# Performance work log

Measured on AMD Instinct MI355X. Metric: run time of the kernel, lower is better.

The kernel has to match this reference:

```python
import jax, jax.numpy as jnp
import numpy as np
from jax import lax

DIM, GC1, GC2, GC3 = 128, 32, 64, 32
B, H, W = 4, 128, 128
EPS = 1e-5


def conv2d(x, w, b, pad, dilation=1, groups=1):
    y = lax.conv_general_dilated(x, w, (1, 1), [(pad, pad), (pad, pad)],
                                 rhs_dilation=(dilation, dilation),
                                 feature_group_count=groups,
                                 dimension_numbers=('NCHW', 'OIHW', 'NCHW'))
    return y + b[None, :, None, None]


def bilinear_gather(img, ys, xs):
    # img [B,C,H,W]; ys,xs [B,K,H,W] float sample coords. Zero padding outside.
    b, c, h, w = img.shape
    k = ys.shape[1]
    flat = img.reshape(b, c, h * w)
    y0 = jnp.floor(ys)
    x0 = jnp.floor(xs)
    acc = jnp.zeros((b, c, k, h, w), img.dtype)
    for dy in (0, 1):
        for dx in (0, 1):
            yc = y0 + dy
            xc = x0 + dx
            wgt = (1.0 - jnp.abs(ys - yc)) * (1.0 - jnp.abs(xs - xc))
            valid = (yc >= 0) & (yc <= h - 1) & (xc >= 0) & (xc <= w - 1)
            yi = jnp.clip(yc, 0, h - 1).astype(jnp.int32)
            xi = jnp.clip(xc, 0, w - 1).astype(jnp.int32)
            idx = (yi * w + xi).reshape(b, 1, k * h * w)
            g = jnp.take_along_axis(flat, jnp.broadcast_to(idx, (b, c, k * h * w)), axis=2)
            g = g.reshape(b, c, k, h, w)
            acc = acc + g * (wgt * valid.astype(img.dtype))[:, None]
    return acc


def deform_depthwise(x, off, w):
    # x [B,C,H,W], off [B,2*9,H,W] (dy,dx interleaved per kernel tap), w [C,9]
    b, c, h, ww = x.shape
    off = off.reshape(b, 9, 2, h, ww)
    dy, dx = off[:, :, 0], off[:, :, 1]  # [B,9,H,W]
    ks = jnp.arange(3, dtype=x.dtype)
    kyy = jnp.repeat(ks, 3)  # [9]
    kxx = jnp.tile(ks, 3)
    iy = jnp.arange(h, dtype=x.dtype)
    jx = jnp.arange(ww, dtype=x.dtype)
    ys = iy[None, None, :, None] - 1.0 + kyy[None, :, None, None] + dy
    xs = jx[None, None, None, :] - 1.0 + kxx[None, :, None, None] + dx
    sampled = bilinear_gather(x, ys, xs)  # [B,C,9,H,W]
    return jnp.einsum('bckhw,ck->bchw', sampled, w)


def batchnorm(x, g, b):
    mu = jnp.mean(x, axis=(0, 2, 3), keepdims=True)
    var = jnp.var(x, axis=(0, 2, 3), keepdims=True)
    return (x - mu) * lax.rsqrt(var + EPS) * g[None, :, None, None] + b[None, :, None, None]


def setup_inputs() -> dict:
    key = jax.random.key(0)
    ks = jax.random.split(key, 16)
    s = 0.05
    return {
        'x': jax.random.normal(ks[0], (B, DIM, H, W), jnp.float32),
        'offset_w': jax.random.normal(ks[1], (18, GC1, 3, 3), jnp.float32) * s,
        'offset_b': jax.random.normal(ks[2], (18,), jnp.float32) * s,
        'deform_w': jax.random.normal(ks[3], (GC1, 9), jnp.float32) * s,
        'dw_w': jax.random.normal(ks[4], (GC2, 1, 7, 7), jnp.float32) * s,
        'dw_b': jax.random.normal(ks[5], (GC2,), jnp.float32) * s,
        'dw2_w': jax.random.normal(ks[6], (GC3, GC3, 3, 3), jnp.float32) * s,
        'dw2_b': jax.random.normal(ks[7], (GC3,), jnp.float32) * s,
        'bn1_g': jnp.ones((DIM,), jnp.float32),
        'bn1_b': jnp.zeros((DIM,), jnp.float32),
        'w1': jax.random.normal(ks[8], (DIM, 4 * DIM), jnp.float32) * s,
        'b1': jax.random.normal(ks[9], (4 * DIM,), jnp.float32) * s,
        'w2': jax.random.normal(ks[10], (4 * DIM, DIM), jnp.float32) * s,
        'b2': jax.random.normal(ks[11], (DIM,), jnp.float32) * s,
        'bn2_g': jnp.ones((DIM,), jnp.float32),
        'bn2_b': jnp.zeros((DIM,), jnp.float32),
    }


def reference(x, offset_w, offset_b, deform_w, dw_w, dw_b, dw2_w, dw2_b,
              bn1_g, bn1_b, w1, b1, w2, b2, bn2_g, bn2_b):
    x_hw, x_w, x_h = jnp.split(x, [GC1, GC1 + GC2], axis=1)
    off = conv2d(x_hw, offset_w, offset_b, pad=1)
    d0 = deform_depthwise(x_hw, off, deform_w)
    d1 = conv2d(x_w, dw_w, dw_b, pad=3, groups=GC2)          # 7x7 depthwise
    d2 = conv2d(x_h, dw2_w, dw2_b, pad=2, dilation=2)        # 3x3 dense, dilation 2
    y = jnp.concatenate([d0, d1, d2], axis=1)
    # channel shuffle, groups=2
    b, c, h, w = y.shape
    y = y.reshape(b, 2, c // 2, h, w).transpose(0, 2, 1, 3, 4).reshape(b, c, h, w)
    y = batchnorm(y, bn1_g, bn1_b)
    t = y.transpose(0, 2, 3, 1)                               # [B,H,W,C]
    t = jax.nn.gelu(t @ w1 + b1, approximate=False)
    t = t @ w2 + b2
    y = t.transpose(0, 3, 1, 2)
    y = batchnorm(y, bn2_g, bn2_b)
    return jax.nn.gelu(x + y, approximate=False)
```

## Files before the change

kernel.cpp:

```cpp
#include <hip/hip_runtime.h>
#include <hip/hip_bf16.h>
#include <math.h>

#define BB 4
#define CC 128
#define HH 128
#define WWD 128
#define HWW 16384
#define PREC 17424

typedef __attribute__((ext_vector_type(8))) short bf16x8;
typedef __attribute__((ext_vector_type(4))) float floatx4;
typedef __attribute__((ext_vector_type(4))) unsigned short us4;
typedef __attribute__((ext_vector_type(8))) unsigned short us8;

__device__ __forceinline__ float gelu_fast(float v) {
  float u = v * v;
  float z = v * fmaf(0.0713548163f, u, 1.5957691216f);
  float e = __builtin_amdgcn_exp2f(-1.4426950409f * z);
  return v * __builtin_amdgcn_rcpf(1.0f + e);
}
__device__ __forceinline__ unsigned short f2us(float f) {
  union { float f; unsigned int u; } c; c.f = f;
  unsigned int u = c.u;
  return (unsigned short)((u + 0x7FFFu + ((u >> 16) & 1u)) >> 16);
}

__global__ __launch_bounds__(256) void k_zero(
    unsigned short* __restrict__ xp, float* __restrict__ part2) {
  if (blockIdx.x == 33) { part2[threadIdx.x] = 0.f; return; }
  int g = blockIdx.x * 256 + threadIdx.x;
  if (g >= 8320) return;
  int pl = g / 1040;
  int r = g - pl * 1040;
  int yy, xx;
  if (r < 528) {
    int q = r / 132;
    yy = q < 2 ? q : 126 + q;
    xx = r - q * 132;
  } else {
    int r2 = r - 528;
    yy = 2 + (r2 >> 2);
    int side = r2 & 3;
    xx = side < 2 ? side : 128 + side;
  }
  long rec = (long)pl * PREC + yy * 132 + xx;
  unsigned short* d = &xp[rec * 32];
  us8 z = (us8)0;
  *(us8*)&d[0] = z; *(us8*)&d[8] = z; *(us8*)&d[16] = z; *(us8*)&d[24] = z;
}

__global__ __launch_bounds__(256) void k_pack(
    const float* __restrict__ x, unsigned short* __restrict__ xp,
    float* __restrict__ xt) {
  __shared__ float t[64 * 33];
  int bid = blockIdx.x;
  int tid = threadIdx.x;
  int which = bid >> 10, b = (bid >> 8) & 3, pg = bid & 255;
  int cbase = which ? 96 : 0;
  int c = tid >> 3, g8 = tid & 7;
  const float* xpr = x + ((long)b * CC + cbase + c) * HWW + pg * 64 + g8 * 8;
  float4 v0 = *(const float4*)xpr;
  float4 v1 = *(const float4*)(xpr + 4);
  t[(g8 * 8 + 0) * 33 + c] = v0.x; t[(g8 * 8 + 1) * 33 + c] = v0.y;
  t[(g8 * 8 + 2) * 33 + c] = v0.z; t[(g8 * 8 + 3) * 33 + c] = v0.w;
  t[(g8 * 8 + 4) * 33 + c] = v1.x; t[(g8 * 8 + 5) * 33 + c] = v1.y;
  t[(g8 * 8 + 6) * 33 + c] = v1.z; t[(g8 * 8 + 7) * 33 + c] = v1.w;
  __syncthreads();
  int u = tid >> 2, q = tid & 3;
  int p = pg * 64 + u;
  int yy = p >> 7, xx = p & 127;
  long rec = (long)(which * 4 + b) * PREC + (yy + 2) * 132 + xx + 2;
  us8 o;
  float vv[8];
#pragma unroll
  for (int k = 0; k < 8; k++) {
    vv[k] = t[u * 33 + q * 8 + k];
    o[k] = f2us(vv[k]);
  }
  *(us8*)&xp[rec * 32 + q * 8] = o;
  if (which == 0) {
    float* d = xt + ((long)b * HWW + p) * 32 + q * 8;
    float4 o0, o1;
    o0.x = vv[0]; o0.y = vv[1]; o0.z = vv[2]; o0.w = vv[3];
    o1.x = vv[4]; o1.y = vv[5]; o1.z = vv[6]; o1.w = vv[7];
    *(float4*)d = o0;
    *(float4*)(d + 4) = o1;
  }
}

__global__ __launch_bounds__(256) void k_wprep2(
    const float* __restrict__ offw, const float* __restrict__ dilw,
    unsigned short* __restrict__ wob, unsigned short* __restrict__ w3b) {
  int t = blockIdx.x * 256 + threadIdx.x;
  if (t >= 2304) return;
  int which = t >= 1152;
  int u = t - which * 1152;
  int lane = u & 63, tn = u >> 6;
  int col = lane & 15, quad = lane >> 4;
  int tap = tn >> 1, nt = tn & 1;
  int n = nt * 16 + col;
  const float* W = which ? dilw : offw;
  int noc = which ? 32 : 18;
  unsigned short* d = (which ? w3b : wob) + (long)(tn * 64 + lane) * 8;
#pragma unroll
  for (int j = 0; j < 8; j++)
    d[j] = (n < noc) ? f2us(W[(long)n * 288 + (quad * 8 + j) * 9 + tap]) : (unsigned short)0;
}

__global__ __launch_bounds__(256) void k_offc_mm(
    const unsigned short* __restrict__ xp0, const unsigned short* __restrict__ wob,
    const float* __restrict__ bias, float* __restrict__ off) {
  int bid = blockIdx.x;
  int b = bid >> 7, yy = bid & 127;
  int tid = threadIdx.x;
  int lane = tid & 63, wv = tid >> 6;
  int row = lane & 15, quad = lane >> 4;
  const unsigned short* plane = xp0 + (long)b * PREC * 32;
  int xb = wv * 32;
  floatx4 Oa[2][2];
#pragma unroll
  for (int mt = 0; mt < 2; mt++)
#pragma unroll
    for (int nt = 0; nt < 2; nt++) Oa[mt][nt] = (floatx4)0.f;
#pragma unroll
  for (int t = 0; t < 9; t++) {
    int dy = t / 3 - 1, dx = t % 3 - 1;
    const unsigned short* rp = plane + ((long)(yy + 2 + dy) * 132 + 2 + dx + xb) * 32;
    bf16x8 A0 = *(const bf16x8*)&rp[row * 32 + quad * 8];
    bf16x8 A1 = *(const bf16x8*)&rp[(16 + row) * 32 + quad * 8];
#pragma unroll
    for (int nt = 0; nt < 2; nt++) {
      bf16x8 Bf = *(const bf16x8*)&wob[(long)((t * 2 + nt) * 64 + lane) * 8];
      Oa[0][nt] = __builtin_amdgcn_mfma_f32_16x16x32_bf16(A0, Bf, Oa[0][nt], 0, 0, 0);
      Oa[1][nt] = __builtin_amdgcn_mfma_f32_16x16x32_bf16(A1, Bf, Oa[1][nt], 0, 0, 0);
    }
  }
#pragma unroll
  for (int nt = 0; nt < 2; nt++) {
    int oc = nt * 16 + (lane & 15);
    if (oc < 18) {
      float bb = bias[oc];
#pragma unroll
      for (int mt = 0; mt < 2; mt++) {
        floatx4 v = Oa[mt][nt];
        v[0] += bb; v[1] += bb; v[2] += bb; v[3] += bb;
        long p = (long)(b * 18 + oc) * HWW + yy * 128 + xb + mt * 16 + quad * 4;
        *(floatx4*)&off[p] = v;
      }
    }
  }
}

__global__ __launch_bounds__(256) void k_dil3_mm(
    const unsigned short* __restrict__ xp1, const unsigned short* __restrict__ w3b,
    const float* __restrict__ bias, float* __restrict__ y) {
  int bid = blockIdx.x;
  int b = bid >> 7, yy = bid & 127;
  int tid = threadIdx.x;
  int lane = tid & 63, wv = tid >> 6;
  int row = lane & 15, quad = lane >> 4;
  const unsigned short* plane = xp1 + (long)b * PREC * 32;
  int xb = wv * 32;
  floatx4 Oa[2][2];
#pragma unroll
  for (int mt = 0; mt < 2; mt++)
#pragma unroll
    for (int nt = 0; nt < 2; nt++) Oa[mt][nt] = (floatx4)0.f;
#pragma unroll
  for (int t = 0; t < 9; t++) {
    int dy = (t / 3 - 1) * 2, dx = (t % 3 - 1) * 2;
    const unsigned short* rp = plane + ((long)(yy + 2 + dy) * 132 + 2 + dx + xb) * 32;
    bf16x8 A0 = *(const bf16x8*)&rp[row * 32 + quad * 8];
    bf16x8 A1 = *(const bf16x8*)&rp[(16 + row) * 32 + quad * 8];
#pragma unroll
    for (int nt = 0; nt < 2; nt++) {
      bf16x8 Bf = *(const bf16x8*)&w3b[(long)((t * 2 + nt) * 64 + lane) * 8];
      Oa[0][nt] = __builtin_amdgcn_mfma_f32_16x16x32_bf16(A0, Bf, Oa[0][nt], 0, 0, 0);
      Oa[1][nt] = __builtin_amdgcn_mfma_f32_16x16x32_bf16(A1, Bf, Oa[1][nt], 0, 0, 0);
    }
  }
#pragma unroll
  for (int nt = 0; nt < 2; nt++) {
    int oc = nt * 16 + (lane & 15);
    int cp = 65 + 2 * oc;
    float bb = bias[oc];
#pragma unroll
    for (int mt = 0; mt < 2; mt++) {
      floatx4 v = Oa[mt][nt];
      v[0] += bb; v[1] += bb; v[2] += bb; v[3] += bb;
      long p = ((long)b * CC + cp) * HWW + yy * 128 + xb + mt * 16 + quad * 4;
      *(floatx4*)&y[p] = v;
    }
  }
}

__global__ __launch_bounds__(256) void k_deform(
    const float* __restrict__ xt, const float* __restrict__ off,
    const float* __restrict__ dw, float* __restrict__ y) {
  __shared__ float wl[144];
  int tid = threadIdx.x;
  int g = blockIdx.x * 256 + tid;
  int hf = g >> 16;
  int pix = g & 65535;
  if (tid < 144) {
    int k = tid >> 4, q = tid & 15;
    wl[k * 16 + q] = dw[(hf * 16 + q) * 9 + k];
  }
  __syncthreads();
  int b = pix >> 14, p = pix & 16383;
  int i = p >> 7, j = p & 127;
  float acc[16];
#pragma unroll
  for (int q = 0; q < 16; q++) acc[q] = 0.f;
  const float* offb = off + (long)b * 18 * HWW + p;
  const float* xb = xt + (long)b * HWW * 32 + hf * 16;
  for (int k = 0; k < 9; k++) {
    float dy = offb[(long)(2 * k) * HWW];
    float dx = offb[(long)(2 * k + 1) * HWW];
    float ys = (float)i - 1.f + (float)(k / 3) + dy;
    float xs = (float)j - 1.f + (float)(k % 3) + dx;
    float y0 = floorf(ys), x0 = floorf(xs);
    float fy = ys - y0, fx = xs - x0;
    int iy0 = (int)y0, ix0 = (int)x0;
    int iy1 = iy0 + 1, ix1 = ix0 + 1;
    float wy0 = (1.f - fy) * ((iy0 >= 0 && iy0 <= 127) ? 1.f : 0.f);
    float wy1 = fy * ((iy1 >= 0 && iy1 <= 127) ? 1.f : 0.f);
    float wx0 = (1.f - fx) * ((ix0 >= 0 && ix0 <= 127) ? 1.f : 0.f);
    float wx1 = fx * ((ix1 >= 0 && ix1 <= 127) ? 1.f : 0.f);
    int cy0 = min(max(iy0, 0), 127), cy1 = min(max(iy1, 0), 127);
    int cx0 = min(max(ix0, 0), 127), cx1 = min(max(ix1, 0), 127);
    int ci[4] = {cy0 * 128 + cx0, cy0 * 128 + cx1, cy1 * 128 + cx0, cy1 * 128 + cx1};
    float cw[4] = {wy0 * wx0, wy0 * wx1, wy1 * wx0, wy1 * wx1};
    float v[16];
#pragma unroll
    for (int q = 0; q < 16; q++) v[q] = 0.f;
#pragma unroll
    for (int cn = 0; cn < 4; cn++) {
      const float* cp = xb + (long)ci[cn] * 32;
      float wc = cw[cn];
      float4 p0 = *(const float4*)cp;
      float4 p1 = *(const float4*)(cp + 4);
      float4 p2 = *(const float4*)(cp + 8);
      float4 p3 = *(const float4*)(cp + 12);
      v[0] += wc * p0.x;  v[1] += wc * p0.y;  v[2] += wc * p0.z;  v[3] += wc * p0.w;
      v[4] += wc * p1.x;  v[5] += wc * p1.y;  v[6] += wc * p1.z;  v[7] += wc * p1.w;
      v[8] += wc * p2.x;  v[9] += wc * p2.y;  v[10] += wc * p2.z; v[11] += wc * p2.w;
      v[12] += wc * p3.x; v[13] += wc * p3.y; v[14] += wc * p3.z; v[15] += wc * p3.w;
    }
    const float* wr = &wl[k * 16];
#pragma unroll
    for (int q = 0; q < 16; q++) acc[q] += wr[q] * v[q];
  }
#pragma unroll
  for (int q = 0; q < 16; q++) {
    int cp = 2 * (hf * 16 + q);
    y[((long)b * CC + cp) * HWW + p] = acc[q];
  }
}

__global__ __launch_bounds__(256) void k_dw7(
    const float* __restrict__ x, const float* __restrict__ w,
    const float* __restrict__ bias, float* __restrict__ y) {
  __shared__ float tile[22 * 136];
  __shared__ float wl[49];
  __shared__ float bsh;
  int bid = blockIdx.x;
  int b = bid >> 9, m = (bid >> 3) & 63, strip = bid & 7;
  int r0 = strip * 16;
  int tid = threadIdx.x;
  const float* xp = x + ((long)b * CC + 32 + m) * HWW;
  for (int idx = tid; idx < 2948; idx += 256) {
    int rr = idx / 134;
    int cc = idx - rr * 134 - 3;
    int gy = r0 - 3 + rr;
    float v = 0.f;
    if ((unsigned)gy < 128u && (unsigned)cc < 128u) v = xp[gy * 128 + cc];
    tile[rr * 136 + cc + 3] = v;
  }
  if (tid < 49) wl[tid] = w[m * 49 + tid];
  if (tid == 64) bsh = bias[m];
  __syncthreads();
  int j = tid & 127, s = tid >> 7;
  float acc[8];
#pragma unroll
  for (int o = 0; o < 8; o++) acc[o] = bsh;
#pragma unroll
  for (int kx = 0; kx < 7; kx++) {
#pragma unroll
    for (int rr = 0; rr < 14; rr++) {
      float v = tile[(s * 8 + rr) * 136 + j + kx];
      int olo = rr - 6 > 0 ? rr - 6 : 0;
      int ohi = rr < 7 ? rr : 7;
#pragma unroll
      for (int o = 0; o < 8; o++) {
        if (o >= olo && o <= ohi) acc[o] += v * wl[(rr - o) * 7 + kx];
      }
    }
  }
  int c = 32 + m;
  int cp = (c & 63) * 2 + (c >> 6);
  float* yp = y + ((long)b * CC + cp) * HWW;
#pragma unroll
  for (int o = 0; o < 8; o++) {
    yp[(r0 + s * 8 + o) * 128 + j] = acc[o];
  }
}

__global__ __launch_bounds__(256) void k_stats1(
    const float* __restrict__ buf, float* __restrict__ part) {
  __shared__ float sh[256], sh2[256];
  int c = blockIdx.x >> 2, b = blockIdx.x & 3;
  int tid = threadIdx.x;
  const float* p = buf + ((long)b * CC + c) * HWW;
  float s = 0.f, s2 = 0.f;
  for (int it = 0; it < 16; it++) {
    float4 v = *(const float4*)(p + (it * 256 + tid) * 4);
    s += v.x + v.y + v.z + v.w;
    s2 += v.x * v.x + v.y * v.y + v.z * v.z + v.w * v.w;
  }
  sh[tid] = s; sh2[tid] = s2;
  __syncthreads();
  for (int o = 128; o > 0; o >>= 1) {
    if (tid < o) { sh[tid] += sh[tid + o]; sh2[tid] += sh2[tid + o]; }
    __syncthreads();
  }
  if (tid == 0) {
    part[blockIdx.x * 2] = sh[0];
    part[blockIdx.x * 2 + 1] = sh2[0];
  }
}

__global__ __launch_bounds__(128) void k_stats2(
    const float* __restrict__ part, float* __restrict__ mean, float* __restrict__ istd) {
  int c = threadIdx.x;
  float s = 0.f, s2 = 0.f;
#pragma unroll
  for (int b = 0; b < 4; b++) {
    s += part[(c * 4 + b) * 2];
    s2 += part[(c * 4 + b) * 2 + 1];
  }
  float mu = s * (1.f / 65536.f);
  float var = s2 * (1.f / 65536.f) - mu * mu;
  mean[c] = mu;
  istd[c] = rsqrtf(var + 1e-5f);
}

__global__ __launch_bounds__(128) void k_stats2b(
    const float* __restrict__ part2, float* __restrict__ mean, float* __restrict__ istd) {
  int c = threadIdx.x;
  float mu = part2[c] * (1.f / 65536.f);
  float var = part2[128 + c] * (1.f / 65536.f) - mu * mu;
  mean[c] = mu;
  istd[c] = rsqrtf(var + 1e-5f);
}

__global__ __launch_bounds__(256) void k_wprep(
    const float* __restrict__ w1, const float* __restrict__ w2,
    unsigned short* __restrict__ w1b, unsigned short* __restrict__ w2b) {
  int t = blockIdx.x * 256 + threadIdx.x;
  int which = t >> 13;
  int u = t & 8191;
  int lane = u & 63;
  int ntks = u >> 6;
  int col = lane & 15, quad = lane >> 4;
  if (which == 0) {
    int nt = ntks >> 2, ks = ntks & 3;
    int n = nt * 16 + col;
    int k0 = ks * 32 + quad * 8;
    unsigned short* d = w1b + (long)u * 8;
#pragma unroll
    for (int j = 0; j < 8; j++) d[j] = f2us(w1[(long)(k0 + j) * 512 + n]);
  } else {
    int nt = ntks >> 4, ks = ntks & 15;
    int n = nt * 16 + col;
    int k0 = ks * 32 + quad * 8;
    unsigned short* d = w2b + (long)u * 8;
#pragma unroll
    for (int j = 0; j < 8; j++) d[j] = f2us(w2[(long)(k0 + j) * 128 + n]);
  }
}

__global__ __launch_bounds__(256, 2) void k_mlp_mfma(
    const float* __restrict__ y, const float* __restrict__ mean1,
    const float* __restrict__ istd1, const float* __restrict__ g1,
    const float* __restrict__ b1n, const unsigned short* __restrict__ w1b,
    const float* __restrict__ b1, const unsigned short* __restrict__ w2b,
    const float* __restrict__ b2, float* __restrict__ tmid,
    float* __restrict__ part2) {
  __shared__ unsigned short At[128 * 136];
  __shared__ unsigned short Hs[4 * 32 * 72];
  __shared__ float scs[128], shs[128];
  __shared__ float ps[128], ps2[128];
  int tid = threadIdx.x;
  int lane = tid & 63, wv = tid >> 6;
  int row = lane & 15, quad = lane >> 4;
  int n0 = blockIdx.x * 128;
  int b = n0 >> 14;
  long base = (long)b * CC * HWW + (n0 & 16383);
  if (tid < 128) {
    float sc = istd1[tid] * g1[tid];
    scs[tid] = sc;
    shs[tid] = b1n[tid] - mean1[tid] * sc;
    ps[tid] = 0.f; ps2[tid] = 0.f;
  }
  __syncthreads();
  for (int it = 0; it < 16; it++) {
    int u = it * 256 + tid;
    int tok = u & 127, cg = u >> 7;
    us4 wvv;
#pragma unroll
    for (int r = 0; r < 4; r++) {
      int c = cg * 4 + r;
      float v = y[base + (long)c * HWW + tok];
      wvv[r] = f2us(v * scs[c] + shs[c]);
    }
    *(us4*)&At[tok * 136 + cg * 4] = wvv;
  }
  __syncthreads();
  bf16x8 Af[2][4];
#pragma unroll
  for (int mt = 0; mt < 2; mt++)
#pragma unroll
    for (int ks = 0; ks < 4; ks++)
      Af[mt][ks] = *(const bf16x8*)&At[(wv * 32 + mt * 16 + row) * 136 + ks * 32 + quad * 8];

  floatx4 Oa[2][8];
#pragma unroll
  for (int mt = 0; mt < 2; mt++)
#pragma unroll
    for (int nt = 0; nt < 8; nt++) Oa[mt][nt] = (floatx4)0.f;

  const int wvb = wv * 32 * 72;
  for (int ch = 0; ch < 8; ch++) {
    floatx4 Ha[4][2];
#pragma unroll
    for (int nt = 0; nt < 4; nt++)
#pragma unroll
      for (int mt = 0; mt < 2; mt++) Ha[nt][mt] = (floatx4)0.f;
#pragma unroll
    for (int nt = 0; nt < 4; nt++) {
      int ht = ch * 4 + nt;
#pragma unroll
      for (int ks = 0; ks < 4; ks++) {
        bf16x8 Wf = *(const bf16x8*)&w1b[(long)(((ht * 4 + ks) << 6) + lane) * 8];
        Ha[nt][0] = __builtin_amdgcn_mfma_f32_16x16x32_bf16(Wf, Af[0][ks], Ha[nt][0], 0, 0, 0);
        Ha[nt][1] = __builtin_amdgcn_mfma_f32_16x16x32_bf16(Wf, Af[1][ks], Ha[nt][1], 0, 0, 0);
      }
    }
#pragma unroll
    for (int nt = 0; nt < 4; nt++) {
      float4 bb = *(const float4*)&b1[ch * 64 + nt * 16 + quad * 4];
#pragma unroll
      for (int mt = 0; mt < 2; mt++) {
        us4 hv;
        hv[0] = f2us(gelu_fast(Ha[nt][mt][0] + bb.x));
        hv[1] = f2us(gelu_fast(Ha[nt][mt][1] + bb.y));
        hv[2] = f2us(gelu_fast(Ha[nt][mt][2] + bb.z));
        hv[3] = f2us(gelu_fast(Ha[nt][mt][3] + bb.w));
        *(us4*)&Hs[wvb + (mt * 16 + row) * 72 + nt * 16 + quad * 4] = hv;
      }
    }
    __syncthreads();
    bf16x8 A2[2][2];
#pragma unroll
    for (int mt = 0; mt < 2; mt++)
#pragma unroll
      for (int ks = 0; ks < 2; ks++)
        A2[mt][ks] = *(const bf16x8*)&Hs[wvb + (mt * 16 + row) * 72 + ks * 32 + quad * 8];
#pragma unroll
    for (int nt = 0; nt < 8; nt++) {
#pragma unroll
      for (int ks = 0; ks < 2; ks++) {
        bf16x8 Bf = *(const bf16x8*)&w2b[(long)(((nt * 16 + ch * 2 + ks) << 6) + lane) * 8];
        Oa[0][nt] = __builtin_amdgcn_mfma_f32_16x16x32_bf16(A2[0][ks], Bf, Oa[0][nt], 0, 0, 0);
        Oa[1][nt] = __builtin_amdgcn_mfma_f32_16x16x32_bf16(A2[1][ks], Bf, Oa[1][nt], 0, 0, 0);
      }
    }
    __syncthreads();
  }
#pragma unroll
  for (int nt = 0; nt < 8; nt++) {
    int c = nt * 16 + row;
    float bb = b2[c];
    long op = base + (long)c * HWW + wv * 32 + quad * 4;
    float s = 0.f, s2 = 0.f;
#pragma unroll
    for (int mt = 0; mt < 2; mt++) {
      floatx4 vv = Oa[mt][nt];
      vv[0] += bb; vv[1] += bb; vv[2] += bb; vv[3] += bb;
      *(floatx4*)&tmid[op + mt * 16] = vv;
      s += vv[0] + vv[1] + vv[2] + vv[3];
      s2 += vv[0] * vv[0] + vv[1] * vv[1] + vv[2] * vv[2] + vv[3] * vv[3];
    }
    atomicAdd(&ps[c], s);
    atomicAdd(&ps2[c], s2);
  }
  __syncthreads();
  if (tid < 128) {
    atomicAdd(&part2[tid], ps[tid]);
    atomicAdd(&part2[128 + tid], ps2[tid]);
  }
}

__global__ __launch_bounds__(256) void k_final(
    const float* __restrict__ x, const float* __restrict__ mean2,
    const float* __restrict__ istd2, const float* __restrict__ g2,
    const float* __restrict__ b2n, float* __restrict__ out) {
  long e4 = (long)blockIdx.x * 256 + threadIdx.x;
  int c = (int)((e4 >> 12) & 127);
  float sc = istd2[c] * g2[c];
  float sh = b2n[c] - mean2[c] * sc;
  float4 o = *(float4*)&out[e4 * 4];
  float4 xv = *(const float4*)&x[e4 * 4];
  o.x = gelu_fast(xv.x + o.x * sc + sh);
  o.y = gelu_fast(xv.y + o.y * sc + sh);
  o.z = gelu_fast(xv.z + o.z * sc + sh);
  o.w = gelu_fast(xv.w + o.w * sc + sh);
  *(float4*)&out[e4 * 4] = o;
}

extern "C" void kernel_launch(void* const* d_in, const int* in_sizes, int n_in,
                              void* d_out, int out_size, void* d_ws, size_t ws_size,
                              hipStream_t stream) {
  const float* x        = (const float*)d_in[0];
  const float* offset_w = (const float*)d_in[1];
  const float* offset_b = (const float*)d_in[2];
  const float* deform_w = (const float*)d_in[3];
  const float* dw_w     = (const float*)d_in[4];
  const float* dw_b     = (const float*)d_in[5];
  const float* dw2_w    = (const float*)d_in[6];
  const float* dw2_b    = (const float*)d_in[7];
  const float* bn1_g    = (const float*)d_in[8];
  const float* bn1_b    = (const float*)d_in[9];
  const float* w1       = (const float*)d_in[10];
  const float* b1       = (const float*)d_in[11];
  const float* w2       = (const float*)d_in[12];
  const float* b2       = (const float*)d_in[13];
  const float* bn2_g    = (const float*)d_in[14];
  const float* bn2_b    = (const float*)d_in[15];
  float* out = (float*)d_out;

  float* ws    = (float*)d_ws;
  float* off   = ws;
  float* ybuf  = ws + 1179648;
  float* stats = ws + 9568256;
  float* mean1 = stats, *istd1 = stats + 128;
  float* mean2 = stats + 256, *istd2 = stats + 384;
  unsigned short* w1b = (unsigned short*)(ws + 9568768);
  unsigned short* w2b = (unsigned short*)(ws + 9601536);
  float* part  = ws + 9634304;
  float* xt    = ws + 9635328;
  unsigned short* wob = (unsigned short*)(ws + 11732480);
  unsigned short* w3b = (unsigned short*)(ws + 11737088);
  unsigned short* xp  = (unsigned short*)(ws + 11741696);
  unsigned short* xp0 = xp;
  unsigned short* xp1 = xp + (long)4 * PREC * 32;
  float* part2 = ws + 13971968;
  float* tmid  = out;

  k_zero<<<34, 256, 0, stream>>>(xp, part2);
  k_wprep<<<64, 256, 0, stream>>>(w1, w2, w1b, w2b);
  k_wprep2<<<9, 256, 0, stream>>>(offset_w, dw2_w, wob, w3b);
  k_pack<<<2048, 256, 0, stream>>>(x, xp, xt);
  k_offc_mm<<<512, 256, 0, stream>>>(xp0, wob, offset_b, off);
  k_deform<<<512, 256, 0, stream>>>(xt, off, deform_w, ybuf);
  k_dw7<<<2048, 256, 0, stream>>>(x, dw_w, dw_b, ybuf);
  k_dil3_mm<<<512, 256, 0, stream>>>(xp1, w3b, dw2_b, ybuf);
  k_stats1<<<512, 256, 0, stream>>>(ybuf, part);
  k_stats2<<<1, 128, 0, stream>>>(part, mean1, istd1);
  k_mlp_mfma<<<512, 256, 0, stream>>>(ybuf, mean1, istd1, bn1_g, bn1_b, w1b, b1, w2b, b2, tmid, part2);
  k_stats2b<<<1, 128, 0, stream>>>(part2, mean2, istd2);
  k_final<<<8192, 256, 0, stream>>>(x, mean2, istd2, bn2_g, bn2_b, out);
}
```

Baseline: 278.8 us.

## Split fused MLP kernel into two GEMM kernels with bf16 hidden buffer

Replaces the single fused MLP kernel (both GEMMs with the hidden activation kept in shared memory) with two kernels. The first writes GELU(W1·BN1(y)) to a global bf16 buffer and the second reads it to compute W2 and the BN2 partial stats. This is meant to lower register and LDS pressure per kernel and raise occupancy with smaller 64-token tiles. The cost is an extra 16 MB write and read of the hidden activation, plus a dependency on workspace size, with a fallback to the fused kernel when the workspace is too small.

```diff
diff --git a/kernel.cpp b/kernel.cpp
--- a/kernel.cpp
+++ b/kernel.cpp
@@ -381,6 +381,115 @@
   }
 }
 
+__global__ __launch_bounds__(256) void k_gemm1(
+    const float* __restrict__ y, const float* __restrict__ mean1,
+    const float* __restrict__ istd1, const float* __restrict__ g1,
+    const float* __restrict__ b1n, const unsigned short* __restrict__ w1b,
+    const float* __restrict__ b1, unsigned short* __restrict__ Hbuf) {
+  __shared__ unsigned short At[64 * 136];
+  __shared__ float scs[128], shs[128];
+  int tid = threadIdx.x;
+  int lane = tid & 63, wv = tid >> 6;
+  int row = lane & 15, quad = lane >> 4;
+  int t0 = blockIdx.x * 64;
+  int b = t0 >> 14;
+  long base = (long)b * CC * HWW + (t0 & 16383);
+  if (tid < 128) {
+    float sc = istd1[tid] * g1[tid];
+    scs[tid] = sc;
+    shs[tid] = b1n[tid] - mean1[tid] * sc;
+  }
+  __syncthreads();
+  for (int it = 0; it < 8; it++) {
+    int u = it * 256 + tid;
+    int tok = u & 63, cg = u >> 6;
+    us4 wvv;
+#pragma unroll
+    for (int r = 0; r < 4; r++) {
+      int c = cg * 4 + r;
+      float v = y[base + (long)c * HWW + tok];
+      wvv[r] = f2us(v * scs[c] + shs[c]);
+    }
+    *(us4*)&At[tok * 136 + cg * 4] = wvv;
+  }
+  __syncthreads();
+  bf16x8 Af[4];
+#pragma unroll
+  for (int ks = 0; ks < 4; ks++)
+    Af[ks] = *(const bf16x8*)&At[(wv * 16 + row) * 136 + ks * 32 + quad * 8];
+  long hrow = ((long)(t0 + wv * 16 + row)) * 512;
+  for (int ch = 0; ch < 8; ch++) {
+    floatx4 Ha[4];
+#pragma unroll
+    for (int nt = 0; nt < 4; nt++) Ha[nt] = (floatx4)0.f;
+#pragma unroll
+    for (int nt = 0; nt < 4; nt++) {
+      int ht = ch * 4 + nt;
+#pragma unroll
+      for (int ks = 0; ks < 4; ks++) {
+        bf16x8 Wf = *(const bf16x8*)&w1b[(long)(((ht * 4 + ks) << 6) + lane) * 8];
+        Ha[nt] = __builtin_amdgcn_mfma_f32_16x16x32_bf16(Wf, Af[ks], Ha[nt], 0, 0, 0);
+      }
+    }
+#pragma unroll
+    for (int nt = 0; nt < 4; nt++) {
+      float4 bb = *(const float4*)&b1[ch * 64 + nt * 16 + quad * 4];
+      us4 hv;
+      hv[0] = f2us(gelu_fast(Ha[nt][0] + bb.x));
+      hv[1] = f2us(gelu_fast(Ha[nt][1] + bb.y));
+      hv[2] = f2us(gelu_fast(Ha[nt][2] + bb.z));
+      hv[3] = f2us(gelu_fast(Ha[nt][3] + bb.w));
+      *(us4*)&Hbuf[hrow + ch * 64 + nt * 16 + quad * 4] = hv;
+    }
+  }
+}
+
+__global__ __launch_bounds__(256) void k_gemm2(
+    const unsigned short* __restrict__ Hbuf, const unsigned short* __restrict__ w2b,
+    const float* __restrict__ b2, float* __restrict__ tmid,
+    float* __restrict__ part2) {
+  __shared__ float ps[128], ps2[128];
+  int tid = threadIdx.x;
+  int lane = tid & 63, wv = tid >> 6;
+  int row = lane & 15, quad = lane >> 4;
+  int t0 = blockIdx.x * 64;
+  int b = t0 >> 14;
+  long base = (long)b * CC * HWW + (t0 & 16383);
+  if (tid < 128) { ps[tid] = 0.f; ps2[tid] = 0.f; }
+  __syncthreads();
+  floatx4 Oa[8];
+#pragma unroll
+  for (int nt = 0; nt < 8; nt++) Oa[nt] = (floatx4)0.f;
+  const unsigned short* hrow = &Hbuf[((long)(t0 + wv * 16 + row)) * 512 + quad * 8];
+#pragma unroll
+  for (int ks = 0; ks < 16; ks++) {
+    bf16x8 A2 = *(const bf16x8*)&hrow[ks * 32];
+#pragma unroll
+    for (int nt = 0; nt < 8; nt++) {
+      bf16x8 Bf = *(const bf16x8*)&w2b[(long)(((nt * 16 + ks) << 6) + lane) * 8];
+      Oa[nt] = __builtin_amdgcn_mfma_f32_16x16x32_bf16(A2, Bf, Oa[nt], 0, 0, 0);
+    }
+  }
+#pragma unroll
+  for (int nt = 0; nt < 8; nt++) {
+    int c = nt * 16 + row;
+    float bb = b2[c];
+    long op = base + (long)c * HWW + wv * 16 + quad * 4;
+    floatx4 vv = Oa[nt];
+    vv[0] += bb; vv[1] += bb; vv[2] += bb; vv[3] += bb;
+    *(floatx4*)&tmid[op] = vv;
+    float s = vv[0] + vv[1] + vv[2] + vv[3];
+    float s2 = vv[0] * vv[0] + vv[1] * vv[1] + vv[2] * vv[2] + vv[3] * vv[3];
+    atomicAdd(&ps[c], s);
+    atomicAdd(&ps2[c], s2);
+  }
+  __syncthreads();
+  if (tid < 128) {
+    atomicAdd(&part2[tid], ps[tid]);
+    atomicAdd(&part2[128 + tid], ps2[tid]);
+  }
+}
+
 __global__ __launch_bounds__(256, 2) void k_mlp_mfma(
     const float* __restrict__ y, const float* __restrict__ mean1,
     const float* __restrict__ istd1, const float* __restrict__ g1,
@@ -557,7 +666,10 @@
   unsigned short* xp0 = xp;
   unsigned short* xp1 = xp + (long)4 * PREC * 32;
   float* part2 = ws + 13971968;
+  unsigned short* Hbuf = (unsigned short*)(ws + 13972224);
   float* tmid  = out;
+  const size_t ws_need = ((size_t)13972224 + 16777216) * 4;
+  int use_split = (ws_size >= ws_need);
 
   k_zero<<<34, 256, 0, stream>>>(xp, part2);
   k_wprep<<<64, 256, 0, stream>>>(w1, w2, w1b, w2b);
@@ -569,7 +681,12 @@
   k_dil3_mm<<<512, 256, 0, stream>>>(xp1, w3b, dw2_b, ybuf);
   k_stats1<<<512, 256, 0, stream>>>(ybuf, part);
   k_stats2<<<1, 128, 0, stream>>>(part, mean1, istd1);
-  k_mlp_mfma<<<512, 256, 0, stream>>>(ybuf, mean1, istd1, bn1_g, bn1_b, w1b, b1, w2b, b2, tmid, part2);
+  if (use_split) {
+    k_gemm1<<<1024, 256, 0, stream>>>(ybuf, mean1, istd1, bn1_g, bn1_b, w1b, b1, Hbuf);
+    k_gemm2<<<1024, 256, 0, stream>>>(Hbuf, w2b, b2, tmid, part2);
+  } else {
+    k_mlp_mfma<<<512, 256, 0, stream>>>(ybuf, mean1, istd1, bn1_g, bn1_b, w1b, b1, w2b, b2, tmid, part2);
+  }
   k_stats2b<<<1, 128, 0, stream>>>(part2, mean2, istd2);
   k_final<<<8192, 256, 0, stream>>>(x, mean2, istd2, bn2_g, bn2_b, out);
 }
```

Result: slower. 305.0 us (+9.4%).
